# Optimization experiments

Hardware: AMD Instinct MI355X
Metric: run time of the kernel (lower is better)

The kernel has to match this reference:

```python
import jax, jax.numpy as jnp
import numpy as np

N = 16384   # flat token count
D = 256     # d_model
M = 64      # median_size (attention in_features / hidden_features)
OUT = 1     # output_size


def setup_inputs() -> dict:
    key = jax.random.key(0)
    ks = jax.random.split(key, 12)
    sD = 1.0 / np.sqrt(D)
    sM = 1.0 / np.sqrt(M)
    rn = lambda k, shape, s: (jax.random.normal(k, shape, jnp.float32) * s)
    return {
        "x":    rn(ks[0], (N, D), 1.0),
        "W1":   rn(ks[1], (D, M), sD), "b1": jnp.zeros((M,), jnp.float32),
        # 3 stacked attention blocks
        "Wq":   rn(ks[2], (3, M, M), sM), "bq": jnp.zeros((3, M), jnp.float32),
        "Wk":   rn(ks[3], (3, M, M), sM), "bk": jnp.zeros((3, M), jnp.float32),
        "Wv":   rn(ks[4], (3, M, M), sM), "bv": jnp.zeros((3, M), jnp.float32),
        "Wf1":  rn(ks[5], (3, M, M), sM), "bf1": jnp.zeros((3, M), jnp.float32),
        "Wf2":  rn(ks[6], (3, M, M), sM), "bf2": jnp.zeros((3, M), jnp.float32),
        "ln_g": jnp.ones((3, M), jnp.float32), "ln_b": jnp.zeros((3, M), jnp.float32),
        "Wout": rn(ks[7], (M, OUT), sM), "bout": jnp.zeros((OUT,), jnp.float32),
    }


def leaky(x, slope):
    return jnp.where(x >= 0, x, slope * x)


def layer_norm(x, g, b, eps=1e-5):
    mu = jnp.mean(x, axis=-1, keepdims=True)
    var = jnp.mean((x - mu) ** 2, axis=-1, keepdims=True)
    return (x - mu) * jax.lax.rsqrt(var + eps) * g + b


def attn_block(x, Wq, bq, Wk, bk, Wv, bv, Wf1, bf1, Wf2, bf2):
    # per-token outer-product attention: attn[n] = softmax(q[n] k[n]^T) over last dim
    q = x @ Wq + bq            # [N, M]
    k = x @ Wk + bk
    v = x @ Wv + bv
    a = jax.nn.softmax(q[:, :, None] * k[:, None, :], axis=-1)   # [N, M, M]
    y = jnp.einsum('nij,nj->ni', a, v) + x                       # residual add (x += x0)
    h = leaky(y @ Wf1 + bf1, 0.01)                               # LeakyReLU(0.01)
    h = h @ Wf2 + bf2
    return h + y                                                 # pred=False residual


def reference(x, W1, b1, Wq, bq, Wk, bk, Wv, bv, Wf1, bf1, Wf2, bf2, ln_g, ln_b, Wout, bout):
    h = x @ W1 + b1                 # Linear_1
    res = leaky(h, 0.1)             # x1 = LeakyReLU(0.1)(h)
    cur = h                         # transformer_1 is applied to pre-activation h
    for t in range(3):
        a = attn_block(cur, Wq[t], bq[t], Wk[t], bk[t], Wv[t], bv[t],
                       Wf1[t], bf1[t], Wf2[t], bf2[t])
        a = layer_norm(a, ln_g[t], ln_b[t])
        res = a + res               # x2 = LN(...) + x1, etc.
        cur = res
    out = leaky(res @ Wout + bout, 0.1).reshape(-1, OUT)
    return (out, out, out, out, out)
```

## Files before the change

### kernel.cpp

```cpp
#include <hip/hip_runtime.h>

#define NTOK 16384
#define TB 16

typedef float f32x4_t __attribute__((ext_vector_type(4)));
typedef short s16x8_t __attribute__((ext_vector_type(8)));

__device__ __forceinline__ unsigned short f2bf(float f) {
    unsigned int x = __float_as_uint(f);
    x += 0x7fffu + ((x >> 16) & 1u);
    return (unsigned short)(x >> 16);
}
__device__ __forceinline__ float fexp2(float x) {
#if __has_builtin(__builtin_amdgcn_exp2f)
    return __builtin_amdgcn_exp2f(x);
#else
    return exp2f(x);
#endif
}
__device__ __forceinline__ float frcp(float x) {
#if __has_builtin(__builtin_amdgcn_rcpf)
    return __builtin_amdgcn_rcpf(x);
#else
    return 1.0f / x;
#endif
}
__device__ __forceinline__ float frsq(float x) {
#if __has_builtin(__builtin_amdgcn_rsqf)
    return __builtin_amdgcn_rsqf(x);
#else
    return rsqrtf(x);
#endif
}

__global__ __launch_bounds__(256)
void prep_kernel(const float* __restrict__ W1,
                 const float* __restrict__ Wq, const float* __restrict__ Wk,
                 const float* __restrict__ Wv, const float* __restrict__ Wf1,
                 const float* __restrict__ Wf2, unsigned short* __restrict__ wsb)
{
    const int i = blockIdx.x * 256 + threadIdx.x;
    if (i < 16384) {
        const int m = i >> 8, k = i & 255;
        wsb[i] = f2bf(W1[k * 64 + m]);
    } else if (i < 77824) {
        const int u  = i - 16384;
        const int mi = u >> 12;
        const int st = mi / 5, q = mi % 5;
        const int r  = u & 4095;
        const int m  = r >> 6, k = r & 63;
        const float* src = q == 0 ? Wq : q == 1 ? Wk : q == 2 ? Wv : q == 3 ? Wf1 : Wf2;
        wsb[i] = f2bf(src[st * 4096 + k * 64 + m]);
    }
}

__global__ __launch_bounds__(256, 4)
void tf3_kernel(const float* __restrict__ x,
                const float* __restrict__ b1,
                const float* __restrict__ bq, const float* __restrict__ bk,
                const float* __restrict__ bv,
                const float* __restrict__ bf1, const float* __restrict__ bf2,
                const float* __restrict__ lng, const float* __restrict__ lnb,
                const float* __restrict__ Wout, const float* __restrict__ bout,
                const unsigned short* __restrict__ wsb,
                float* __restrict__ out)
{
    __shared__ __align__(16) unsigned short w3_lds[3 * 4096];
    __shared__ __align__(16) unsigned short a_lds[16 * 64];
    __shared__ __align__(16) float q_lds[16 * 68];
    __shared__ __align__(16) float ky_lds[16 * 68];
    __shared__ __align__(16) float v_lds[16 * 68];

    const int tid = threadIdx.x;
    const int wv  = tid >> 6;
    const int l   = tid & 63;
    const int n0  = blockIdx.x * TB;

    const int lr  = l & 15;
    const int q4  = l >> 4;
    const int c   = wv * 16 + lr;

    const int g  = q4;
    const int e  = lr;
    const int tg = wv * 4 + g;

    float res_reg[4], cur_reg[4];

    auto LOAD2 = [&](int matIdx, s16x8_t& r0, s16x8_t& r1) {
        const char* gb = (const char*)(wsb + 16384 + matIdx * 4096) + wv * 2048 + l * 16;
        r0 = *reinterpret_cast<const s16x8_t*>(gb);
        r1 = *reinterpret_cast<const s16x8_t*>(gb + 1024);
    };
    auto WRITE2 = [&](int slot, s16x8_t r0, s16x8_t r1) {
        #pragma unroll
        for (int p = 0; p < 2; ++p) {
            const int b  = wv * 2048 + p * 1024 + l * 16;
            const int mm = b >> 7;
            const int sw = ((b >> 4) & 7) ^ (mm & 7);
            *reinterpret_cast<s16x8_t*>((char*)w3_lds + slot * 8192 + (b & ~127) + (sw << 4))
                = p ? r1 : r0;
        }
    };
    auto mm16 = [&](s16x8_t af0, s16x8_t af1, const unsigned short* bbase) -> f32x4_t {
        const s16x8_t b0  = *reinterpret_cast<const s16x8_t*>(&bbase[c * 64 + (((0 + q4) ^ (c & 7)) * 8)]);
        const s16x8_t b1f = *reinterpret_cast<const s16x8_t*>(&bbase[c * 64 + (((4 + q4) ^ (c & 7)) * 8)]);
        f32x4_t acc = __builtin_amdgcn_mfma_f32_16x16x32_bf16(af0, b0, (f32x4_t){0.f,0.f,0.f,0.f}, 0, 0, 0);
        acc = __builtin_amdgcn_mfma_f32_16x16x32_bf16(af1, b1f, acc, 0, 0, 0);
        return acc;
    };

    s16x8_t wr0, wr1, wr2, wr3, wr4, wr5;

    LOAD2(0, wr0, wr1); LOAD2(1, wr2, wr3); LOAD2(2, wr4, wr5);

    {
        const float* xrow = x + (size_t)(n0 + lr) * 256;
        f32x4_t acch = {0.f, 0.f, 0.f, 0.f};
        #pragma unroll
        for (int s5 = 0; s5 < 8; ++s5) {
            const int k0 = s5 * 32 + q4 * 8;
            const float4 u0 = *reinterpret_cast<const float4*>(xrow + k0);
            const float4 u1 = *reinterpret_cast<const float4*>(xrow + k0 + 4);
            s16x8_t af;
            af[0] = (short)f2bf(u0.x); af[1] = (short)f2bf(u0.y);
            af[2] = (short)f2bf(u0.z); af[3] = (short)f2bf(u0.w);
            af[4] = (short)f2bf(u1.x); af[5] = (short)f2bf(u1.y);
            af[6] = (short)f2bf(u1.z); af[7] = (short)f2bf(u1.w);
            const s16x8_t bf = *reinterpret_cast<const s16x8_t*>(&wsb[c * 256 + k0]);
            acch = __builtin_amdgcn_mfma_f32_16x16x32_bf16(af, bf, acch, 0, 0, 0);
        }
        const float bb = b1[c];
        #pragma unroll
        for (int rg = 0; rg < 4; ++rg)
            q_lds[(q4 * 4 + rg) * 68 + c] = acch[rg] + bb;
    }
    WRITE2(0, wr0, wr1); WRITE2(1, wr2, wr3); WRITE2(2, wr4, wr5);
    __syncthreads();
    #pragma unroll
    for (int tt = 0; tt < 4; ++tt) {
        const int t = wv * 4 + tt;
        const float h = q_lds[t * 68 + l];
        cur_reg[tt] = h;
        res_reg[tt] = h >= 0.f ? h : 0.1f * h;
        a_lds[t * 64 + (((l >> 3) ^ (t & 7)) * 8) + (l & 7)] = f2bf(h);
    }

    for (int st = 0; st < 3; ++st) {
        const float bqv  = bq[st * 64 + c];
        const float bkv  = bk[st * 64 + c];
        const float bvv  = bv[st * 64 + c];
        const float bf1v = bf1[st * 64 + c];
        const float bf2v = bf2[st * 64 + c];
        const float lngv = lng[st * 64 + l];
        const float lnbv = lnb[st * 64 + l];

        __syncthreads();
        {
            const s16x8_t af0 = *reinterpret_cast<const s16x8_t*>(&a_lds[lr * 64 + ((q4       ^ (lr & 7)) * 8)]);
            const s16x8_t af1 = *reinterpret_cast<const s16x8_t*>(&a_lds[lr * 64 + (((4 + q4) ^ (lr & 7)) * 8)]);
            f32x4_t aq = mm16(af0, af1, &w3_lds[0]);
            f32x4_t ak = mm16(af0, af1, &w3_lds[4096]);
            f32x4_t av = mm16(af0, af1, &w3_lds[8192]);
            #pragma unroll
            for (int rg = 0; rg < 4; ++rg) {
                const int tr = q4 * 4 + rg;
                q_lds[tr * 68 + c]  = aq[rg] + bqv;
                ky_lds[tr * 68 + c] = ak[rg] + bkv;
                v_lds[tr * 68 + c]  = av[rg] + bvv;
            }
        }
        LOAD2(st * 5 + 3, wr0, wr1);
        LOAD2(st * 5 + 4, wr2, wr3);
        __syncthreads();

        float kmax_t[4], kmin_t[4];
        {
            const float4 kv = *reinterpret_cast<const float4*>(&ky_lds[tg * 68 + e * 4]);
            float kmx = fmaxf(fmaxf(kv.x, kv.y), fmaxf(kv.z, kv.w));
            float kmn = fminf(fminf(kv.x, kv.y), fminf(kv.z, kv.w));
            #pragma unroll
            for (int m = 1; m < 16; m <<= 1) {
                kmx = fmaxf(kmx, __shfl_xor(kmx, m, 64));
                kmn = fminf(kmn, __shfl_xor(kmn, m, 64));
            }
            #pragma unroll
            for (int tt = 0; tt < 4; ++tt) {
                kmax_t[tt] = __shfl(kmx, tt * 16, 64);
                kmin_t[tt] = __shfl(kmn, tt * 16, 64);
            }
        }
        #pragma unroll
        for (int tt = 0; tt < 4; ++tt) {
            const int t = wv * 4 + tt;
            const float qs = q_lds[t * 68 + l] * 1.44269504088896340736f;
            const float m2 = fmaxf(qs * kmax_t[tt], qs * kmin_t[tt]);
            float s0 = 0.f, s1 = 0.f, p0 = 0.f, p1 = 0.f;
            #pragma unroll
            for (int j = 0; j < 64; j += 4) {
                const float4 kj = *reinterpret_cast<const float4*>(&ky_lds[t * 68 + j]);
                const float4 vj = *reinterpret_cast<const float4*>(&v_lds[t * 68 + j]);
                const float e0 = fexp2(fmaf(qs, kj.x, -m2));
                const float e1 = fexp2(fmaf(qs, kj.y, -m2));
                const float e2v = fexp2(fmaf(qs, kj.z, -m2));
                const float e3 = fexp2(fmaf(qs, kj.w, -m2));
                s0 += e0 + e2v; s1 += e1 + e3;
                p0 = fmaf(e0, vj.x, p0); p1 = fmaf(e1, vj.y, p1);
                p0 = fmaf(e2v, vj.z, p0); p1 = fmaf(e3, vj.w, p1);
            }
            const float y = (p0 + p1) * frcp(s0 + s1) + cur_reg[tt];
            ky_lds[t * 68 + l] = y;
        }
        __syncthreads();

        WRITE2(0, wr0, wr1); WRITE2(1, wr2, wr3);

        {
            f32x4_t acc = {0.f, 0.f, 0.f, 0.f};
            #pragma unroll
            for (int kh = 0; kh < 2; ++kh) {
                const float* yp = &ky_lds[lr * 68 + kh * 32 + q4 * 8];
                const float4 y0 = *reinterpret_cast<const float4*>(yp);
                const float4 y1 = *reinterpret_cast<const float4*>(yp + 4);
                s16x8_t af;
                af[0] = (short)f2bf(y0.x); af[1] = (short)f2bf(y0.y);
                af[2] = (short)f2bf(y0.z); af[3] = (short)f2bf(y0.w);
                af[4] = (short)f2bf(y1.x); af[5] = (short)f2bf(y1.y);
                af[6] = (short)f2bf(y1.z); af[7] = (short)f2bf(y1.w);
                const int ck = kh * 4 + q4;
                const s16x8_t bf = *reinterpret_cast<const s16x8_t*>(&w3_lds[c * 64 + ((ck ^ (c & 7)) * 8)]);
                acc = __builtin_amdgcn_mfma_f32_16x16x32_bf16(af, bf, acc, 0, 0, 0);
            }
            #pragma unroll
            for (int rg = 0; rg < 4; ++rg) {
                const int tr = q4 * 4 + rg;
                float h = acc[rg] + bf1v;
                h = h >= 0.f ? h : 0.01f * h;
                a_lds[tr * 64 + (((c >> 3) ^ (tr & 7)) * 8) + (c & 7)] = f2bf(h);
            }
        }
        if (st < 2) {
            LOAD2((st + 1) * 5 + 0, wr0, wr1);
            LOAD2((st + 1) * 5 + 1, wr2, wr3);
            LOAD2((st + 1) * 5 + 2, wr4, wr5);
        }
        __syncthreads();

        {
            const s16x8_t ag0 = *reinterpret_cast<const s16x8_t*>(&a_lds[lr * 64 + ((q4       ^ (lr & 7)) * 8)]);
            const s16x8_t ag1 = *reinterpret_cast<const s16x8_t*>(&a_lds[lr * 64 + (((4 + q4) ^ (lr & 7)) * 8)]);
            f32x4_t acc = mm16(ag0, ag1, &w3_lds[4096]);
            #pragma unroll
            for (int rg = 0; rg < 4; ++rg) {
                const int tr = q4 * 4 + rg;
                ky_lds[tr * 68 + c] += acc[rg] + bf2v;
            }
        }
        __syncthreads();

        {
            const float4 av4 = *reinterpret_cast<const float4*>(&ky_lds[tg * 68 + e * 4]);
            float ssum = av4.x + av4.y + av4.z + av4.w;
            #pragma unroll
            for (int m = 1; m < 16; m <<= 1) ssum += __shfl_xor(ssum, m, 64);
            const float mug = ssum * 0.015625f;
            const float d0 = av4.x - mug, d1 = av4.y - mug, d2 = av4.z - mug, d3 = av4.w - mug;
            float vsum = d0 * d0 + d1 * d1 + d2 * d2 + d3 * d3;
            #pragma unroll
            for (int m = 1; m < 16; m <<= 1) vsum += __shfl_xor(vsum, m, 64);
            #pragma unroll
            for (int tt = 0; tt < 4; ++tt) {
                const int t = wv * 4 + tt;
                const float mu = __shfl(mug, tt * 16, 64);
                const float vv = __shfl(vsum, tt * 16, 64);
                const float rs = frsq(vv * 0.015625f + 1e-5f);
                const float a  = ky_lds[t * 68 + l];
                const float an = (a - mu) * rs * lngv + lnbv;
                const float rnew = res_reg[tt] + an;
                res_reg[tt] = rnew;
                cur_reg[tt] = rnew;
                a_lds[t * 64 + (((l >> 3) ^ (t & 7)) * 8) + (l & 7)] = f2bf(rnew);
            }
        }
        if (st < 2) { WRITE2(0, wr0, wr1); WRITE2(1, wr2, wr3); WRITE2(2, wr4, wr5); }
    }

    const float wo = Wout[l];
    const float bo = bout[0];
    #pragma unroll
    for (int tt = 0; tt < 4; ++tt)
        q_lds[(wv * 4 + tt) * 68 + l] = res_reg[tt] * wo;
    {
        const float4 pv = *reinterpret_cast<const float4*>(&q_lds[tg * 68 + e * 4]);
        float p = pv.x + pv.y + pv.z + pv.w;
        #pragma unroll
        for (int m = 1; m < 16; m <<= 1) p += __shfl_xor(p, m, 64);
        if (e == 0) {
            float o = p + bo;
            o = o >= 0.f ? o : 0.1f * o;
            #pragma unroll
            for (int c5 = 0; c5 < 5; ++c5)
                out[(size_t)c5 * NTOK + n0 + tg] = o;
        }
    }
}

extern "C" void kernel_launch(void* const* d_in, const int* in_sizes, int n_in,
                              void* d_out, int out_size, void* d_ws, size_t ws_size,
                              hipStream_t stream) {
    const float* x    = (const float*)d_in[0];
    const float* W1   = (const float*)d_in[1];
    const float* b1   = (const float*)d_in[2];
    const float* Wq   = (const float*)d_in[3];
    const float* bq   = (const float*)d_in[4];
    const float* Wk   = (const float*)d_in[5];
    const float* bk   = (const float*)d_in[6];
    const float* Wv   = (const float*)d_in[7];
    const float* bv   = (const float*)d_in[8];
    const float* Wf1  = (const float*)d_in[9];
    const float* bf1  = (const float*)d_in[10];
    const float* Wf2  = (const float*)d_in[11];
    const float* bf2  = (const float*)d_in[12];
    const float* lngp = (const float*)d_in[13];
    const float* lnbp = (const float*)d_in[14];
    const float* Wout = (const float*)d_in[15];
    const float* bout = (const float*)d_in[16];
    float* outp = (float*)d_out;
    unsigned short* wsb = (unsigned short*)d_ws;

    hipLaunchKernelGGL(prep_kernel, dim3(304), dim3(256), 0, stream,
                       W1, Wq, Wk, Wv, Wf1, Wf2, wsb);
    hipLaunchKernelGGL(tf3_kernel, dim3(NTOK / TB), dim3(256), 0, stream,
                       x, b1, bq, bk, bv, bf1, bf2, lngp, lnbp, Wout, bout,
                       (const unsigned short*)wsb, outp);
}
```

Baseline: 64.88 us.

## Stage x tile in LDS as bf16, use packed bf16 converts, software-pipeline softmax loads

Before Linear_1, each block now loads the x tile cooperatively with coalesced float4 reads and converts it with the hardware packed bf16 instruction. It writes the result to a swizzled LDS region and feeds the MFMA from there. Before this, every wave reloaded the full x rows redundantly from global memory. The bf16 conversions in the attention and FFN paths also switch to v_cvt_pk_bf16_f32, replacing the manual rounding, and the softmax inner loop prefetches the next k and v chunk into registers. The change adds an extra barrier and raises register pressure.

```diff
diff --git a/kernel.cpp b/kernel.cpp
--- a/kernel.cpp
+++ b/kernel.cpp
@@ -6,7 +6,19 @@
 typedef float f32x4_t __attribute__((ext_vector_type(4)));
 typedef short s16x8_t __attribute__((ext_vector_type(8)));
 
+union bfpack { unsigned int u[4]; s16x8_t v; };
+
+__device__ __forceinline__ unsigned int pk2bf(float lo, float hi) {
+    unsigned int r;
+    asm("v_cvt_pk_bf16_f32 %0, %1, %2" : "=v"(r) : "v"(lo), "v"(hi));
+    return r;
+}
 __device__ __forceinline__ unsigned short f2bf(float f) {
+    unsigned int r;
+    asm("v_cvt_pk_bf16_f32 %0, %1, %1" : "=v"(r) : "v"(f));
+    return (unsigned short)r;
+}
+__device__ __forceinline__ unsigned short f2bf_host_style(float f) {
     unsigned int x = __float_as_uint(f);
     x += 0x7fffu + ((x >> 16) & 1u);
     return (unsigned short)(x >> 16);
@@ -42,7 +54,7 @@
     const int i = blockIdx.x * 256 + threadIdx.x;
     if (i < 16384) {
         const int m = i >> 8, k = i & 255;
-        wsb[i] = f2bf(W1[k * 64 + m]);
+        wsb[i] = f2bf_host_style(W1[k * 64 + m]);
     } else if (i < 77824) {
         const int u  = i - 16384;
         const int mi = u >> 12;
@@ -50,7 +62,7 @@
         const int r  = u & 4095;
         const int m  = r >> 6, k = r & 63;
         const float* src = q == 0 ? Wq : q == 1 ? Wk : q == 2 ? Wv : q == 3 ? Wf1 : Wf2;
-        wsb[i] = f2bf(src[st * 4096 + k * 64 + m]);
+        wsb[i] = f2bf_host_style(src[st * 4096 + k * 64 + m]);
     }
 }
 
@@ -80,9 +92,8 @@
     const int q4  = l >> 4;
     const int c   = wv * 16 + lr;
 
-    const int g  = q4;
-    const int e  = lr;
-    const int tg = wv * 4 + g;
+    const int ge = lr;
+    const int tg = wv * 4 + q4;
 
     float res_reg[4], cur_reg[4];
 
@@ -114,19 +125,31 @@
     LOAD2(0, wr0, wr1); LOAD2(1, wr2, wr3); LOAD2(2, wr4, wr5);
 
     {
-        const float* xrow = x + (size_t)(n0 + lr) * 256;
+        const int r  = tid & 15;
+        const int cb = tid >> 4;
+        const float* xp = x + (size_t)(n0 + r) * 256 + cb * 16;
+        const float4 u0 = *reinterpret_cast<const float4*>(xp);
+        const float4 u1 = *reinterpret_cast<const float4*>(xp + 4);
+        const float4 u2 = *reinterpret_cast<const float4*>(xp + 8);
+        const float4 u3 = *reinterpret_cast<const float4*>(xp + 12);
+        bfpack P0, P1;
+        P0.u[0] = pk2bf(u0.x, u0.y); P0.u[1] = pk2bf(u0.z, u0.w);
+        P0.u[2] = pk2bf(u1.x, u1.y); P0.u[3] = pk2bf(u1.z, u1.w);
+        P1.u[0] = pk2bf(u2.x, u2.y); P1.u[1] = pk2bf(u2.z, u2.w);
+        P1.u[2] = pk2bf(u3.x, u3.y); P1.u[3] = pk2bf(u3.z, u3.w);
+        char* rowb = (char*)w3_lds + r * 512;
+        *reinterpret_cast<s16x8_t*>(rowb + (((cb * 2    ) ^ (r & 7)) << 4)) = P0.v;
+        *reinterpret_cast<s16x8_t*>(rowb + (((cb * 2 + 1) ^ (r & 7)) << 4)) = P1.v;
+    }
+    __syncthreads();
+
+    {
         f32x4_t acch = {0.f, 0.f, 0.f, 0.f};
         #pragma unroll
         for (int s5 = 0; s5 < 8; ++s5) {
-            const int k0 = s5 * 32 + q4 * 8;
-            const float4 u0 = *reinterpret_cast<const float4*>(xrow + k0);
-            const float4 u1 = *reinterpret_cast<const float4*>(xrow + k0 + 4);
-            s16x8_t af;
-            af[0] = (short)f2bf(u0.x); af[1] = (short)f2bf(u0.y);
-            af[2] = (short)f2bf(u0.z); af[3] = (short)f2bf(u0.w);
-            af[4] = (short)f2bf(u1.x); af[5] = (short)f2bf(u1.y);
-            af[6] = (short)f2bf(u1.z); af[7] = (short)f2bf(u1.w);
-            const s16x8_t bf = *reinterpret_cast<const s16x8_t*>(&wsb[c * 256 + k0]);
+            const s16x8_t af = *reinterpret_cast<const s16x8_t*>(
+                (const char*)w3_lds + lr * 512 + ((((s5 * 4 + q4)) ^ (lr & 7)) << 4));
+            const s16x8_t bf = *reinterpret_cast<const s16x8_t*>(&wsb[c * 256 + s5 * 32 + q4 * 8]);
             acch = __builtin_amdgcn_mfma_f32_16x16x32_bf16(af, bf, acch, 0, 0, 0);
         }
         const float bb = b1[c];
@@ -134,8 +157,8 @@
         for (int rg = 0; rg < 4; ++rg)
             q_lds[(q4 * 4 + rg) * 68 + c] = acch[rg] + bb;
     }
+    __syncthreads();
     WRITE2(0, wr0, wr1); WRITE2(1, wr2, wr3); WRITE2(2, wr4, wr5);
-    __syncthreads();
     #pragma unroll
     for (int tt = 0; tt < 4; ++tt) {
         const int t = wv * 4 + tt;
@@ -175,7 +198,7 @@
 
         float kmax_t[4], kmin_t[4];
         {
-            const float4 kv = *reinterpret_cast<const float4*>(&ky_lds[tg * 68 + e * 4]);
+            const float4 kv = *reinterpret_cast<const float4*>(&ky_lds[tg * 68 + ge * 4]);
             float kmx = fmaxf(fmaxf(kv.x, kv.y), fmaxf(kv.z, kv.w));
             float kmn = fminf(fminf(kv.x, kv.y), fminf(kv.z, kv.w));
             #pragma unroll
@@ -194,18 +217,31 @@
             const int t = wv * 4 + tt;
             const float qs = q_lds[t * 68 + l] * 1.44269504088896340736f;
             const float m2 = fmaxf(qs * kmax_t[tt], qs * kmin_t[tt]);
+            const float* kb = &ky_lds[t * 68];
+            const float* vb = &v_lds[t * 68];
+            float4 ka0 = *reinterpret_cast<const float4*>(kb);
+            float4 ka1 = *reinterpret_cast<const float4*>(kb + 4);
+            float4 va0 = *reinterpret_cast<const float4*>(vb);
+            float4 va1 = *reinterpret_cast<const float4*>(vb + 4);
             float s0 = 0.f, s1 = 0.f, p0 = 0.f, p1 = 0.f;
             #pragma unroll
-            for (int j = 0; j < 64; j += 4) {
-                const float4 kj = *reinterpret_cast<const float4*>(&ky_lds[t * 68 + j]);
-                const float4 vj = *reinterpret_cast<const float4*>(&v_lds[t * 68 + j]);
-                const float e0 = fexp2(fmaf(qs, kj.x, -m2));
-                const float e1 = fexp2(fmaf(qs, kj.y, -m2));
-                const float e2v = fexp2(fmaf(qs, kj.z, -m2));
-                const float e3 = fexp2(fmaf(qs, kj.w, -m2));
-                s0 += e0 + e2v; s1 += e1 + e3;
-                p0 = fmaf(e0, vj.x, p0); p1 = fmaf(e1, vj.y, p1);
-                p0 = fmaf(e2v, vj.z, p0); p1 = fmaf(e3, vj.w, p1);
+            for (int j = 0; j < 64; j += 8) {
+                float4 kn0, kn1, vn0, vn1;
+                if (j < 56) {
+                    kn0 = *reinterpret_cast<const float4*>(kb + j + 8);
+                    kn1 = *reinterpret_cast<const float4*>(kb + j + 12);
+                    vn0 = *reinterpret_cast<const float4*>(vb + j + 8);
+                    vn1 = *reinterpret_cast<const float4*>(vb + j + 12);
+                }
+                const float e0 = fexp2(fmaf(qs, ka0.x, -m2)); s0 += e0; p0 = fmaf(e0, va0.x, p0);
+                const float e1 = fexp2(fmaf(qs, ka0.y, -m2)); s1 += e1; p1 = fmaf(e1, va0.y, p1);
+                const float e2 = fexp2(fmaf(qs, ka0.z, -m2)); s0 += e2; p0 = fmaf(e2, va0.z, p0);
+                const float e3 = fexp2(fmaf(qs, ka0.w, -m2)); s1 += e3; p1 = fmaf(e3, va0.w, p1);
+                const float e4 = fexp2(fmaf(qs, ka1.x, -m2)); s0 += e4; p0 = fmaf(e4, va1.x, p0);
+                const float e5 = fexp2(fmaf(qs, ka1.y, -m2)); s1 += e5; p1 = fmaf(e5, va1.y, p1);
+                const float e6 = fexp2(fmaf(qs, ka1.z, -m2)); s0 += e6; p0 = fmaf(e6, va1.z, p0);
+                const float e7 = fexp2(fmaf(qs, ka1.w, -m2)); s1 += e7; p1 = fmaf(e7, va1.w, p1);
+                ka0 = kn0; ka1 = kn1; va0 = vn0; va1 = vn1;
             }
             const float y = (p0 + p1) * frcp(s0 + s1) + cur_reg[tt];
             ky_lds[t * 68 + l] = y;
@@ -221,14 +257,12 @@
                 const float* yp = &ky_lds[lr * 68 + kh * 32 + q4 * 8];
                 const float4 y0 = *reinterpret_cast<const float4*>(yp);
                 const float4 y1 = *reinterpret_cast<const float4*>(yp + 4);
-                s16x8_t af;
-                af[0] = (short)f2bf(y0.x); af[1] = (short)f2bf(y0.y);
-                af[2] = (short)f2bf(y0.z); af[3] = (short)f2bf(y0.w);
-                af[4] = (short)f2bf(y1.x); af[5] = (short)f2bf(y1.y);
-                af[6] = (short)f2bf(y1.z); af[7] = (short)f2bf(y1.w);
+                bfpack P;
+                P.u[0] = pk2bf(y0.x, y0.y); P.u[1] = pk2bf(y0.z, y0.w);
+                P.u[2] = pk2bf(y1.x, y1.y); P.u[3] = pk2bf(y1.z, y1.w);
                 const int ck = kh * 4 + q4;
                 const s16x8_t bf = *reinterpret_cast<const s16x8_t*>(&w3_lds[c * 64 + ((ck ^ (c & 7)) * 8)]);
-                acc = __builtin_amdgcn_mfma_f32_16x16x32_bf16(af, bf, acc, 0, 0, 0);
+                acc = __builtin_amdgcn_mfma_f32_16x16x32_bf16(P.v, bf, acc, 0, 0, 0);
             }
             #pragma unroll
             for (int rg = 0; rg < 4; ++rg) {
@@ -258,7 +292,7 @@
         __syncthreads();
 
         {
-            const float4 av4 = *reinterpret_cast<const float4*>(&ky_lds[tg * 68 + e * 4]);
+            const float4 av4 = *reinterpret_cast<const float4*>(&ky_lds[tg * 68 + ge * 4]);
             float ssum = av4.x + av4.y + av4.z + av4.w;
             #pragma unroll
             for (int m = 1; m < 16; m <<= 1) ssum += __shfl_xor(ssum, m, 64);
@@ -290,11 +324,11 @@
     for (int tt = 0; tt < 4; ++tt)
         q_lds[(wv * 4 + tt) * 68 + l] = res_reg[tt] * wo;
     {
-        const float4 pv = *reinterpret_cast<const float4*>(&q_lds[tg * 68 + e * 4]);
+        const float4 pv = *reinterpret_cast<const float4*>(&q_lds[tg * 68 + ge * 4]);
         float p = pv.x + pv.y + pv.z + pv.w;
         #pragma unroll
         for (int m = 1; m < 16; m <<= 1) p += __shfl_xor(p, m, 64);
-        if (e == 0) {
+        if (ge == 0) {
             float o = p + bo;
             o = o >= 0.f ? o : 0.1f * o;
             #pragma unroll
```

Result: faster. 57.40 us (-11.5%).
